# Performance work log

Hardware: AMD Instinct MI355X
Metric: run time of the kernel (lower is better)

The kernel has to match this reference:

```python
import jax, jax.numpy as jnp
import numpy as np

S, B, HID, NH = 256, 2, 512, 8
HD = HID // NH
C = 1.0            # Poincare ball curvature c (geoopt k = -c)
SQC = C ** 0.5
EPS = 1e-15


def _artanh(x):
    return jnp.arctanh(jnp.clip(x, -1 + 1e-7, 1 - 1e-7))


def artan_k(x):
    return _artanh(SQC * x) / SQC


def tan_k(x):
    return jnp.tanh(SQC * x) / SQC


def mobius_add(x, y):
    x2 = jnp.sum(x * x, -1, keepdims=True)
    y2 = jnp.sum(y * y, -1, keepdims=True)
    xy = jnp.sum(x * y, -1, keepdims=True)
    num = (1 + 2 * C * xy + C * y2) * x + (1 - C * x2) * y
    den = 1 + 2 * C * xy + C * C * x2 * y2
    return num / jnp.maximum(den, EPS)


def mobius_matvec(W, x):
    x_norm = jnp.maximum(jnp.linalg.norm(x, axis=-1, keepdims=True), EPS)
    mx = x @ W.T
    mx_norm = jnp.maximum(jnp.linalg.norm(mx, axis=-1, keepdims=True), EPS)
    res = tan_k(mx_norm / x_norm * artan_k(x_norm)) * (mx / mx_norm)
    zero = jnp.all(mx == 0, axis=-1, keepdims=True)
    return jnp.where(zero, 0.0, res)


def projx(x):
    n = jnp.maximum(jnp.linalg.norm(x, axis=-1, keepdims=True), EPS)
    maxnorm = (1 - 4e-3) / SQC  # float32 eps in geoopt
    return jnp.where(n > maxnorm, x / n * maxnorm, x)


def expmap0(u):
    n = jnp.maximum(jnp.linalg.norm(u, axis=-1, keepdims=True), EPS)
    return tan_k(n) * u / n


def logmap0(y):
    n = jnp.maximum(jnp.linalg.norm(y, axis=-1, keepdims=True), EPS)
    return artan_k(n) * y / n


def mobius_scalar_mul(r, x):
    n = jnp.maximum(jnp.linalg.norm(x, axis=-1, keepdims=True), EPS)
    return tan_k(r * artan_k(n)) * x / n


def manifold_linear(W, b, x):
    return projx(mobius_add(mobius_matvec(W, x), b))


def setup_inputs() -> dict:
    key = jax.random.key(0)
    ks = jax.random.split(key, 7)
    q = jax.random.normal(ks[0], (S, B, HID), jnp.float32) * 0.02
    w = lambda k: jax.random.normal(k, (HID, HID), jnp.float32) * 0.02
    bias = lambda k: jax.random.normal(k, (HID,), jnp.float32) * 0.01
    return {"query": q,
            "Wq": w(ks[1]), "bq": bias(ks[2]),
            "Wk": w(ks[3]), "bk": bias(ks[4]),
            "Wv": w(ks[5]), "bv": bias(ks[6])}


def reference(query, Wq, bq, Wk, bk, Wv, bv):
    x = jnp.transpose(query, (1, 0, 2))  # [B,S,HID], key=value=query
    Bn, Sn, _ = x.shape
    q = manifold_linear(Wq, bq, x)
    k = manifold_linear(Wk, bk, x)
    v = manifold_linear(Wv, bv, x)
    # faithful to torch .view(-1, H, S, D): plain memory reshape (not transpose)
    ql = expmap0(logmap0(q).reshape(Bn, NH, Sn, HD))
    kl = expmap0(logmap0(k).reshape(Bn, NH, Sn, HD))
    vl = expmap0(logmap0(v).reshape(Bn, NH, Sn, HD))
    # pairwise mobius_add(-q, k) -> [B,H,Q,N,D]; torch norm(p=-2) over D (faithful)
    diff = mobius_add(-ql[:, :, :, None, :], kl[:, :, None, :, :])
    t1 = jnp.sum(jnp.maximum(diff * diff, 1e-30) ** -1.0, axis=-1) ** -0.5
    scores = jnp.clip(-2.0 * artan_k(t1), -1e10, 1e10)
    probs = jax.nn.sigmoid(scores)  # [B,H,Q,N]; dropout p=0 -> identity
    # weighted gyro-midpoint over N (geoopt _weighted_midpoint, reducedim=[-1])
    gamma = 2.0 / jnp.maximum(1.0 - C * jnp.sum(vl * vl, -1), EPS)  # [B,H,N]
    denom = jnp.einsum('bhqn,bhn->bhq', probs, gamma - 1.0)
    sgn = jnp.where(denom >= 0, 1.0, -1.0)
    denom = sgn * jnp.maximum(jnp.abs(denom), 1e-10)
    nom = jnp.einsum('bhqn,bhnd->bhqd', probs, gamma[..., None] * vl)
    ctx = mobius_scalar_mul(0.5, nom / denom[..., None])  # [B,H,Q,D]
    ctx = jnp.transpose(ctx, (0, 2, 1, 3))  # [B,Q,H,D]
    ctx = expmap0(logmap0(ctx).reshape(Bn, Sn, HID))
    return jnp.transpose(ctx, (1, 0, 2)), probs
```

## Files before the change

### kernel.cpp

```cpp
#include <hip/hip_runtime.h>
#include <math.h>

constexpr int S_   = 256;
constexpr int B_   = 2;
constexpr int HID_ = 512;
constexpr int NH_  = 8;
constexpr int HD_  = 64;
constexpr int BSH  = B_ * S_ * HID_;


typedef unsigned short u16;
typedef short s16x8 __attribute__((ext_vector_type(8)));
typedef float f32x4 __attribute__((ext_vector_type(4)));

__device__ __forceinline__ float artanh_c(float x) {
    x = fminf(fmaxf(x, -0.9999999f), 0.9999999f);
    return 0.5f * __logf((1.f + x) / (1.f - x));
}

__device__ __forceinline__ float wsum64(float v) {
    #pragma unroll
    for (int o = 1; o < 64; o <<= 1) v += __shfl_xor(v, o, 64);
    return v;
}

__device__ __forceinline__ float block_sum_256(float v, float* red) {
    const int t = threadIdx.x;
    __syncthreads();
    red[t] = v;
    __syncthreads();
    #pragma unroll
    for (int sft = 128; sft > 0; sft >>= 1) {
        if (t < sft) red[t] += red[t + sft];
        __syncthreads();
    }
    return red[0];
}

__device__ __forceinline__ void split8(const float* v, s16x8& hi, s16x8& lo) {
    #pragma unroll
    for (int j = 0; j < 8; ++j) {
        const unsigned u = __float_as_uint(v[j]);
        const float hf = __uint_as_float(u & 0xFFFF0000u);
        hi[j] = (short)(u >> 16);
        lo[j] = (short)(__float_as_uint(v[j] - hf) >> 16);
    }
}

__global__ __launch_bounds__(256) void gemm3_fused_kernel(
    const float* __restrict__ query,
    const float* __restrict__ Wq, const float* __restrict__ Wk,
    const float* __restrict__ Wv, float* __restrict__ ws_mx)
{
    const int tid = threadIdx.x;
    const int rt = blockIdx.x >> 3;
    const int ct = blockIdx.x & 7;
    const int which = (rt * 32) >> 9;
    const int rloc  = (rt * 32) & 511;
    const float* __restrict__ W = (which == 0) ? Wq : (which == 1) ? Wk : Wv;

    __shared__ __align__(16) u16 sA[2][2][32 * 64];
    __shared__ __align__(16) u16 sB[2][2][64 * 64];

    const int ra = tid >> 3, sa = tid & 7;
    const int rb = tid >> 2, hb = (tid & 3) * 2;
    const int axrow = rloc + ra;
    const float* gA = query + (size_t)((axrow & 255) * 2 + (axrow >> 8)) * HID_ + sa * 8;
    const float* gB = W + (size_t)(ct * 64 + rb) * HID_ + hb * 8;
    const int wA  = ra * 64 + ((sa ^ (ra & 7)) * 8);
    const int wB0 = rb * 64 + ((hb ^ (rb & 7)) * 8);
    const int wB1 = rb * 64 + (((hb + 1) ^ (rb & 7)) * 8);

    const int lane = tid & 63, wv = tid >> 6;
    const int fr = lane & 15, fs = lane >> 4;
    const int aB0 = fr * 64,        ax0 = fr & 7;
    const int aB1 = (16 + fr) * 64, ax1 = (16 + fr) & 7;
    const int bB  = (wv * 16 + fr) * 64, bx = (wv * 16 + fr) & 7;

    float a8[8], b16[16];
    f32x4 acc[2] = {(f32x4){0.f,0.f,0.f,0.f}, (f32x4){0.f,0.f,0.f,0.f}};

#define G3_LOAD(c)  do { \
        const int k0 = (c) * 64; \
        *(float4*)&a8[0]  = *(const float4*)(gA + k0); \
        *(float4*)&a8[4]  = *(const float4*)(gA + k0 + 4); \
        *(float4*)&b16[0] = *(const float4*)(gB + k0); \
        *(float4*)&b16[4] = *(const float4*)(gB + k0 + 4); \
        *(float4*)&b16[8] = *(const float4*)(gB + k0 + 8); \
        *(float4*)&b16[12]= *(const float4*)(gB + k0 + 12); \
    } while (0)

#define G3_WRITE(b) do { \
        s16x8 h_, l_; \
        split8(a8, h_, l_); \
        *(s16x8*)&sA[b][0][wA] = h_;  *(s16x8*)&sA[b][1][wA] = l_; \
        split8(&b16[0], h_, l_); \
        *(s16x8*)&sB[b][0][wB0] = h_; *(s16x8*)&sB[b][1][wB0] = l_; \
        split8(&b16[8], h_, l_); \
        *(s16x8*)&sB[b][0][wB1] = h_; *(s16x8*)&sB[b][1][wB1] = l_; \
    } while (0)

    G3_LOAD(0);
    G3_WRITE(0);

    for (int c = 0; c < 8; ++c) {
        const int p = c & 1;
        __syncthreads();
        if (c < 7) G3_LOAD(c + 1);
        #pragma unroll
        for (int h = 0; h < 2; ++h) {
            const int sl = h * 4 + fs;
            s16x8 ah0 = *(const s16x8*)&sA[p][0][aB0 + ((sl ^ ax0) * 8)];
            s16x8 al0 = *(const s16x8*)&sA[p][1][aB0 + ((sl ^ ax0) * 8)];
            s16x8 ah1 = *(const s16x8*)&sA[p][0][aB1 + ((sl ^ ax1) * 8)];
            s16x8 al1 = *(const s16x8*)&sA[p][1][aB1 + ((sl ^ ax1) * 8)];
            s16x8 bh  = *(const s16x8*)&sB[p][0][bB  + ((sl ^ bx)  * 8)];
            s16x8 bl  = *(const s16x8*)&sB[p][1][bB  + ((sl ^ bx)  * 8)];
            acc[0] = __builtin_amdgcn_mfma_f32_16x16x32_bf16(ah0, bh, acc[0], 0, 0, 0);
            acc[0] = __builtin_amdgcn_mfma_f32_16x16x32_bf16(ah0, bl, acc[0], 0, 0, 0);
            acc[0] = __builtin_amdgcn_mfma_f32_16x16x32_bf16(al0, bh, acc[0], 0, 0, 0);
            acc[1] = __builtin_amdgcn_mfma_f32_16x16x32_bf16(ah1, bh, acc[1], 0, 0, 0);
            acc[1] = __builtin_amdgcn_mfma_f32_16x16x32_bf16(ah1, bl, acc[1], 0, 0, 0);
            acc[1] = __builtin_amdgcn_mfma_f32_16x16x32_bf16(al1, bh, acc[1], 0, 0, 0);
        }
        if (c < 7) G3_WRITE((c + 1) & 1);
    }
#undef G3_LOAD
#undef G3_WRITE

    #pragma unroll
    for (int i = 0; i < 2; ++i)
        #pragma unroll
        for (int q = 0; q < 4; ++q)
            ws_mx[(size_t)(rt * 32 + i * 16 + fs * 4 + q) * HID_ + ct * 64 + wv * 16 + fr]
                = acc[i][q];
}

__global__ __launch_bounds__(256) void mobius_rows_kernel(
    const float* __restrict__ query,
    const float* __restrict__ bq, const float* __restrict__ bk,
    const float* __restrict__ bv,
    float* __restrict__ ws_qkv, float* __restrict__ ws_gamma)
{
    const int lane = threadIdx.x & 63;
    const int wv   = threadIdx.x >> 6;
    const int row  = blockIdx.x * 4 + wv;
    const int which = row >> 9;
    const int rr    = row & 511;
    const float* __restrict__ bias = (which == 0) ? bq : (which == 1) ? bk : bv;
    float* mrow = ws_qkv + (size_t)row * HID_;
    const float* xrow = query + (size_t)((rr & 255) * 2 + (rr >> 8)) * HID_;

    float m[8], x[8], bb[8];
    *(float4*)&m[0]  = ((const float4*)mrow)[lane * 2];
    *(float4*)&m[4]  = ((const float4*)mrow)[lane * 2 + 1];
    *(float4*)&x[0]  = ((const float4*)xrow)[lane * 2];
    *(float4*)&x[4]  = ((const float4*)xrow)[lane * 2 + 1];
    *(float4*)&bb[0] = ((const float4*)bias)[lane * 2];
    *(float4*)&bb[4] = ((const float4*)bias)[lane * 2 + 1];

    float x2p = 0.f, m2p = 0.f, b2p = 0.f;
    #pragma unroll
    for (int j = 0; j < 8; ++j) {
        x2p = fmaf(x[j], x[j], x2p);
        m2p = fmaf(m[j], m[j], m2p);
        b2p = fmaf(bb[j], bb[j], b2p);
    }
    const float x2s = wsum64(x2p);
    const float mn2 = wsum64(m2p);
    const float b2s = wsum64(b2p);
    const float xn = fmaxf(sqrtf(x2s), 1e-15f);
    const float mn = fmaxf(sqrtf(mn2), 1e-15f);
    const float fac = tanhf(mn / xn * artanh_c(xn)) / mn;
    float r[8];
    float r2p = 0.f, ryp = 0.f;
    #pragma unroll
    for (int j = 0; j < 8; ++j) {
        r[j] = fac * m[j];
        r2p = fmaf(r[j], r[j], r2p);
        ryp = fmaf(r[j], bb[j], ryp);
    }
    const float r2s = wsum64(r2p);
    const float ry  = wsum64(ryp);
    const float a_c = 1.f + 2.f * ry + b2s;
    const float b_c = 1.f - r2s;
    const float den = 1.f + 2.f * ry + r2s * b2s;
    const float inv_den = 1.f / fmaxf(den, 1e-15f);
    float h[8];
    float h2p = 0.f;
    #pragma unroll
    for (int j = 0; j < 8; ++j) {
        h[j] = (a_c * r[j] + b_c * bb[j]) * inv_den;
        h2p = fmaf(h[j], h[j], h2p);
    }
    const float h2s = wsum64(h2p);
    float hn = fmaxf(sqrtf(h2s), 1e-15f);
    float pf = 1.f;
    if (hn > 0.996f) { pf = 0.996f / hn; hn = 0.996f; }
    const float lf = artanh_c(hn) / hn * pf;
    float l[8];
    float l2p = 0.f;
    #pragma unroll
    for (int j = 0; j < 8; ++j) {
        l[j] = lf * h[j];
        l2p = fmaf(l[j], l[j], l2p);
    }
    float cs = l2p;
    cs += __shfl_xor(cs, 1, 64);
    cs += __shfl_xor(cs, 2, 64);
    cs += __shfl_xor(cs, 4, 64);
    const float cn = fmaxf(sqrtf(cs), 1e-15f);
    const float th = tanhf(cn);
    const float sc = th / cn;
    float o[8];
    #pragma unroll
    for (int j = 0; j < 8; ++j) o[j] = sc * l[j];
    ((float4*)mrow)[lane * 2]     = *(float4*)&o[0];
    ((float4*)mrow)[lane * 2 + 1] = *(float4*)&o[4];
    if (which == 2 && (lane & 7) == 0) {
        const int j = lane >> 3;
        ws_gamma[(size_t)rr * NH_ + j] = 2.f / fmaxf(1.f - th * th, 1e-15f);
    }
}

__global__ __launch_bounds__(512, 4) void attn_kernel(
    const float* __restrict__ ws_qkv, const float* __restrict__ gamma,
    float* __restrict__ probs, float* __restrict__ lc)
{
    const int tid = threadIdx.x;
    const int bh  = blockIdx.x >> 5;
    const int q0  = (blockIdx.x & 31) * 8;
    const float* __restrict__ ql = ws_qkv + (size_t)bh * (S_ * HD_);
    const float* __restrict__ kl = ws_qkv + (size_t)BSH + (size_t)bh * (S_ * HD_);
    const float* __restrict__ vl = ws_qkv + (size_t)2 * BSH + (size_t)bh * (S_ * HD_);

    __shared__ __align__(16) float kS[128 * 64];
    __shared__ __align__(16) float qS[8 * 64];
    __shared__ __align__(16) float pS[8 * 256];
    __shared__ float gS[S_];
    __shared__ float k2S[128];
    __shared__ float nomP[8][8][64];
    __shared__ float dnS[8];

    if (tid < 256) gS[tid] = gamma[(size_t)bh * S_ + tid];
    if (tid < 128) ((float4*)qS)[tid] = ((const float4*)(ql + (size_t)q0 * 64))[tid];
    __syncthreads();

    const int lane = tid & 63;
    const int q_l  = tid >> 6;
    const int n_i  = lane & 31;
    const int dh   = lane >> 5;
    const int d0   = dh * 32;

    float qv[32];
    #pragma unroll
    for (int c = 0; c < 8; ++c)
        *(float4*)&qv[c * 4] = *(const float4*)&qS[q_l * 64 + d0 + c * 4];
    float q2p = 0.f;
    #pragma unroll
    for (int d = 0; d < 32; ++d) q2p = fmaf(qv[d], qv[d], q2p);
    const float q2 = q2p + __shfl_xor(q2p, 32, 64);
    const float b_c = 1.f - q2;
    float* __restrict__ prow = probs + ((size_t)(bh * S_ + q0 + q_l)) * S_;

    const int c4 = tid & 15;
    const int nb = tid >> 4;
    float sp = 0.f, spg = 0.f;

    for (int half = 0; half < 2; ++half) {
        __syncthreads();
        #pragma unroll
        for (int jj = 0; jj < 4; ++jj) {
            const int n = nb + 32 * jj;
            const float4 v = *(const float4*)(kl + ((size_t)(half * 128 + n)) * 64 + c4 * 4);
            *(float4*)&kS[n * 64 + ((c4 ^ (n & 15)) * 4)] = v;
            float pk = fmaf(v.x, v.x, fmaf(v.y, v.y, fmaf(v.z, v.z, v.w * v.w)));
            pk += __shfl_xor(pk, 1, 64);
            pk += __shfl_xor(pk, 2, 64);
            pk += __shfl_xor(pk, 4, 64);
            pk += __shfl_xor(pk, 8, 64);
            if (c4 == 0) k2S[n] = pk;
        }
        __syncthreads();
        #pragma unroll
        for (int j = 0; j < 4; ++j) {
            const int n = n_i + 32 * j;
            float kv[32];
            #pragma unroll
            for (int c = 0; c < 8; ++c) {
                const int sl = dh * 8 + c;
                *(float4*)&kv[c * 4] = *(const float4*)&kS[n * 64 + ((sl ^ (n & 15)) * 4)];
            }
            float s0 = 0.f, s1 = 0.f;
            #pragma unroll
            for (int d = 0; d < 32; d += 2) {
                s0 = fmaf(qv[d],     kv[d],     s0);
                s1 = fmaf(qv[d + 1], kv[d + 1], s1);
            }
            float s = s0 + s1;
            s += __shfl_xor(s, 32, 64);
            const float k2  = k2S[n];
            const float a_c = 1.f - 2.f * s + k2;
            const float den = fmaxf(fmaf(q2, k2, 1.f - 2.f * s), 1e-15f);
            const float ra  = __builtin_amdgcn_rcpf(a_c);
            const float r_c = b_c * ra;
            const float scale = den * den * ra * ra;
            const float c2  = 1e-30f * scale;
            float isA = 0.f, isB = 0.f;
            #pragma unroll
            for (int g = 0; g < 8; g += 2) {
                {
                    const int bse = g * 4;
                    const float w0 = fmaf(r_c, kv[bse + 0], -qv[bse + 0]);
                    const float w1 = fmaf(r_c, kv[bse + 1], -qv[bse + 1]);
                    const float w2 = fmaf(r_c, kv[bse + 2], -qv[bse + 2]);
                    const float w3 = fmaf(r_c, kv[bse + 3], -qv[bse + 3]);
                    const float ga = fmaf(w0, w0, c2), gb = fmaf(w1, w1, c2);
                    const float gc = fmaf(w2, w2, c2), gd = fmaf(w3, w3, c2);
                    const float pab = ga * gb, pcd = gc * gd;
                    const float num = fmaf(ga + gb, pcd, (gc + gd) * pab);
                    isA = fmaf(num, __builtin_amdgcn_rcpf(pab * pcd), isA);
                }
                {
                    const int bse = (g + 1) * 4;
                    const float w0 = fmaf(r_c, kv[bse + 0], -qv[bse + 0]);
                    const float w1 = fmaf(r_c, kv[bse + 1], -qv[bse + 1]);
                    const float w2 = fmaf(r_c, kv[bse + 2], -qv[bse + 2]);
                    const float w3 = fmaf(r_c, kv[bse + 3], -qv[bse + 3]);
                    const float ga = fmaf(w0, w0, c2), gb = fmaf(w1, w1, c2);
                    const float gc = fmaf(w2, w2, c2), gd = fmaf(w3, w3, c2);
                    const float pab = ga * gb, pcd = gc * gd;
                    const float num = fmaf(ga + gb, pcd, (gc + gd) * pab);
                    isB = fmaf(num, __builtin_amdgcn_rcpf(pab * pcd), isB);
                }
            }
            float invsum = isA + isB;
            invsum += __shfl_xor(invsum, 32, 64);
            const float t1 = __builtin_amdgcn_rsqf(scale * invsum);
            const float p = 0.5f - 0.5f * fminf(t1, 0.9999999f);
            const int gn = half * 128 + n;
            if (dh == 0) {
                prow[gn] = p;
                const float g = gS[gn];
                pS[q_l * 256 + gn] = p * g;
                sp += p; spg += p * g;
            }
        }
    }
    sp  = wsum64(sp);
    spg = wsum64(spg);
    if (lane == 0) dnS[q_l] = spg - sp;
    __syncthreads();

    const int w = q_l, d = lane;
    float acc[8] = {};
    const float* __restrict__ vbase = vl + (size_t)(w * 32) * 64;
    #pragma unroll
    for (int i4 = 0; i4 < 8; ++i4) {
        float vv[4];
        #pragma unroll
        for (int j2 = 0; j2 < 4; ++j2) vv[j2] = vbase[(size_t)(i4 * 4 + j2) * 64 + d];
        #pragma unroll
        for (int qq = 0; qq < 8; ++qq) {
            const float4 pq = *(const float4*)&pS[qq * 256 + w * 32 + i4 * 4];
            acc[qq] = fmaf(pq.x, vv[0], acc[qq]);
            acc[qq] = fmaf(pq.y, vv[1], acc[qq]);
            acc[qq] = fmaf(pq.z, vv[2], acc[qq]);
            acc[qq] = fmaf(pq.w, vv[3], acc[qq]);
        }
    }
    #pragma unroll
    for (int qq = 0; qq < 8; ++qq) nomP[w][qq][d] = acc[qq];
    __syncthreads();

    {
        const int qq = q_l;
        float nom = 0.f;
        #pragma unroll
        for (int w2 = 0; w2 < 8; ++w2) nom += nomP[w2][qq][d];
        const float dd = dnS[qq];
        const float adn = fmaxf(fabsf(dd), 1e-10f);
        const float sden = (dd >= 0.f) ? adn : -adn;
        const float m = nom / sden;
        const float ss = wsum64(m * m);
        const float nn = fmaxf(sqrtf(ss), 1e-15f);
        const float s1 = tanhf(0.5f * artanh_c(nn));
        const float res = s1 * m / nn;
        const float nres = fmaxf(s1, 1e-15f);
        lc[((size_t)(bh * S_ + q0 + qq)) * HD_ + d] = (artanh_c(nres) / nres) * res;
    }
}

__global__ __launch_bounds__(256) void outproj_kernel(
    const float* __restrict__ lc, float* __restrict__ out0)
{
    const int t = threadIdx.x;
    const int s = blockIdx.x & (S_ - 1);
    const int b = blockIdx.x >> 8;
    __shared__ float red[256];
    const int h0 = t >> 6, d0 = t & 63;
    const int e1 = t + 256;
    const int h1 = e1 >> 6, d1 = e1 & 63;
    const float v0 = lc[(((size_t)(b * NH_ + h0)) * S_ + s) * HD_ + d0];
    const float v1 = lc[(((size_t)(b * NH_ + h1)) * S_ + s) * HD_ + d1];
    const float ss = block_sum_256(v0 * v0 + v1 * v1, red);
    const float nn = fmaxf(sqrtf(ss), 1e-15f);
    const float f = tanhf(nn) / nn;
    float* orow = out0 + ((size_t)(s * B_ + b)) * HID_;
    orow[t] = f * v0;
    orow[t + 256] = f * v1;
}

extern "C" void kernel_launch(void* const* d_in, const int* in_sizes, int n_in,
                              void* d_out, int out_size, void* d_ws, size_t ws_size,
                              hipStream_t stream) {
    (void)in_sizes; (void)n_in; (void)out_size; (void)ws_size;
    const float* query = (const float*)d_in[0];
    const float* Wq = (const float*)d_in[1];
    const float* bq = (const float*)d_in[2];
    const float* Wk = (const float*)d_in[3];
    const float* bk = (const float*)d_in[4];
    const float* Wv = (const float*)d_in[5];
    const float* bv = (const float*)d_in[6];

    float* out0  = (float*)d_out;
    float* probs = out0 + (size_t)S_ * B_ * HID_;

    float* ws       = (float*)d_ws;
    float* ws_qkv   = ws;
    float* ws_gamma = ws + (size_t)3 * BSH;
    float* ws_lc    = ws + (size_t)3 * BSH + 4096;

    gemm3_fused_kernel<<<dim3(384), dim3(256), 0, stream>>>(query, Wq, Wk, Wv, ws_qkv);
    mobius_rows_kernel<<<dim3(384), dim3(256), 0, stream>>>(query, bq, bk, bv, ws_qkv, ws_gamma);
    attn_kernel<<<dim3(512), dim3(512), 0, stream>>>(ws_qkv, ws_gamma, probs, ws_lc);
    outproj_kernel<<<dim3(B_ * S_), dim3(256), 0, stream>>>(ws_lc, out0);
}
```

Measured before the change: 105.2 us.

## Fuse mobius row epilogue into GEMM and outproj into attention via last-block counters

Replaces the separate mobius_rows and outproj launches with last-arriving-block epilogues: the GEMM block that finishes a row tile's eighth column tile runs the mobius/projection math for those 32 rows. The attention block that completes all eight heads for a query group computes the output normalization. This removes two kernel launches and their inter-kernel gaps, but adds a memset launch, atomics and threadfences, and serializes the epilogue work onto fewer blocks.

Result: slower. 270.0 us (+156.7%).

```diff
diff --git a/kernel.cpp b/kernel.cpp
--- a/kernel.cpp
+++ b/kernel.cpp
@@ -24,19 +24,6 @@
     return v;
 }
 
-__device__ __forceinline__ float block_sum_256(float v, float* red) {
-    const int t = threadIdx.x;
-    __syncthreads();
-    red[t] = v;
-    __syncthreads();
-    #pragma unroll
-    for (int sft = 128; sft > 0; sft >>= 1) {
-        if (t < sft) red[t] += red[t + sft];
-        __syncthreads();
-    }
-    return red[0];
-}
-
 __device__ __forceinline__ void split8(const float* v, s16x8& hi, s16x8& lo) {
     #pragma unroll
     for (int j = 0; j < 8; ++j) {
@@ -47,10 +34,13 @@
     }
 }
 
-__global__ __launch_bounds__(256) void gemm3_fused_kernel(
+__global__ __launch_bounds__(256) void gemm3_mobius_kernel(
     const float* __restrict__ query,
-    const float* __restrict__ Wq, const float* __restrict__ Wk,
-    const float* __restrict__ Wv, float* __restrict__ ws_mx)
+    const float* __restrict__ Wq, const float* __restrict__ bq,
+    const float* __restrict__ Wk, const float* __restrict__ bk,
+    const float* __restrict__ Wv, const float* __restrict__ bv,
+    float* __restrict__ ws_qkv, float* __restrict__ ws_gamma,
+    unsigned int* __restrict__ cnt)
 {
     const int tid = threadIdx.x;
     const int rt = blockIdx.x >> 3;
@@ -61,6 +51,7 @@
 
     __shared__ __align__(16) u16 sA[2][2][32 * 64];
     __shared__ __align__(16) u16 sB[2][2][64 * 64];
+    __shared__ unsigned int lastS;
 
     const int ra = tid >> 3, sa = tid & 7;
     const int rb = tid >> 2, hb = (tid & 3) * 2;
@@ -71,11 +62,11 @@
     const int wB0 = rb * 64 + ((hb ^ (rb & 7)) * 8);
     const int wB1 = rb * 64 + (((hb + 1) ^ (rb & 7)) * 8);
 
-    const int lane = tid & 63, wv = tid >> 6;
+    const int lane = tid & 63, wvg = tid >> 6;
     const int fr = lane & 15, fs = lane >> 4;
     const int aB0 = fr * 64,        ax0 = fr & 7;
     const int aB1 = (16 + fr) * 64, ax1 = (16 + fr) & 7;
-    const int bB  = (wv * 16 + fr) * 64, bx = (wv * 16 + fr) & 7;
+    const int bB  = (wvg * 16 + fr) * 64, bx = (wvg * 16 + fr) & 7;
 
     float a8[8], b16[16];
     f32x4 acc[2] = {(f32x4){0.f,0.f,0.f,0.f}, (f32x4){0.f,0.f,0.f,0.f}};
@@ -132,100 +123,105 @@
     for (int i = 0; i < 2; ++i)
         #pragma unroll
         for (int q = 0; q < 4; ++q)
-            ws_mx[(size_t)(rt * 32 + i * 16 + fs * 4 + q) * HID_ + ct * 64 + wv * 16 + fr]
+            ws_qkv[(size_t)(rt * 32 + i * 16 + fs * 4 + q) * HID_ + ct * 64 + wvg * 16 + fr]
                 = acc[i][q];
-}
-
-__global__ __launch_bounds__(256) void mobius_rows_kernel(
-    const float* __restrict__ query,
-    const float* __restrict__ bq, const float* __restrict__ bk,
-    const float* __restrict__ bv,
-    float* __restrict__ ws_qkv, float* __restrict__ ws_gamma)
-{
-    const int lane = threadIdx.x & 63;
-    const int wv   = threadIdx.x >> 6;
-    const int row  = blockIdx.x * 4 + wv;
-    const int which = row >> 9;
-    const int rr    = row & 511;
-    const float* __restrict__ bias = (which == 0) ? bq : (which == 1) ? bk : bv;
-    float* mrow = ws_qkv + (size_t)row * HID_;
-    const float* xrow = query + (size_t)((rr & 255) * 2 + (rr >> 8)) * HID_;
-
-    float m[8], x[8], bb[8];
-    *(float4*)&m[0]  = ((const float4*)mrow)[lane * 2];
-    *(float4*)&m[4]  = ((const float4*)mrow)[lane * 2 + 1];
-    *(float4*)&x[0]  = ((const float4*)xrow)[lane * 2];
-    *(float4*)&x[4]  = ((const float4*)xrow)[lane * 2 + 1];
-    *(float4*)&bb[0] = ((const float4*)bias)[lane * 2];
-    *(float4*)&bb[4] = ((const float4*)bias)[lane * 2 + 1];
-
-    float x2p = 0.f, m2p = 0.f, b2p = 0.f;
-    #pragma unroll
-    for (int j = 0; j < 8; ++j) {
-        x2p = fmaf(x[j], x[j], x2p);
-        m2p = fmaf(m[j], m[j], m2p);
-        b2p = fmaf(bb[j], bb[j], b2p);
-    }
-    const float x2s = wsum64(x2p);
-    const float mn2 = wsum64(m2p);
-    const float b2s = wsum64(b2p);
-    const float xn = fmaxf(sqrtf(x2s), 1e-15f);
-    const float mn = fmaxf(sqrtf(mn2), 1e-15f);
-    const float fac = tanhf(mn / xn * artanh_c(xn)) / mn;
-    float r[8];
-    float r2p = 0.f, ryp = 0.f;
-    #pragma unroll
-    for (int j = 0; j < 8; ++j) {
-        r[j] = fac * m[j];
-        r2p = fmaf(r[j], r[j], r2p);
-        ryp = fmaf(r[j], bb[j], ryp);
-    }
-    const float r2s = wsum64(r2p);
-    const float ry  = wsum64(ryp);
-    const float a_c = 1.f + 2.f * ry + b2s;
-    const float b_c = 1.f - r2s;
-    const float den = 1.f + 2.f * ry + r2s * b2s;
-    const float inv_den = 1.f / fmaxf(den, 1e-15f);
-    float h[8];
-    float h2p = 0.f;
-    #pragma unroll
-    for (int j = 0; j < 8; ++j) {
-        h[j] = (a_c * r[j] + b_c * bb[j]) * inv_den;
-        h2p = fmaf(h[j], h[j], h2p);
-    }
-    const float h2s = wsum64(h2p);
-    float hn = fmaxf(sqrtf(h2s), 1e-15f);
-    float pf = 1.f;
-    if (hn > 0.996f) { pf = 0.996f / hn; hn = 0.996f; }
-    const float lf = artanh_c(hn) / hn * pf;
-    float l[8];
-    float l2p = 0.f;
-    #pragma unroll
-    for (int j = 0; j < 8; ++j) {
-        l[j] = lf * h[j];
-        l2p = fmaf(l[j], l[j], l2p);
-    }
-    float cs = l2p;
-    cs += __shfl_xor(cs, 1, 64);
-    cs += __shfl_xor(cs, 2, 64);
-    cs += __shfl_xor(cs, 4, 64);
-    const float cn = fmaxf(sqrtf(cs), 1e-15f);
-    const float th = tanhf(cn);
-    const float sc = th / cn;
-    float o[8];
-    #pragma unroll
-    for (int j = 0; j < 8; ++j) o[j] = sc * l[j];
-    ((float4*)mrow)[lane * 2]     = *(float4*)&o[0];
-    ((float4*)mrow)[lane * 2 + 1] = *(float4*)&o[4];
-    if (which == 2 && (lane & 7) == 0) {
-        const int j = lane >> 3;
-        ws_gamma[(size_t)rr * NH_ + j] = 2.f / fmaxf(1.f - th * th, 1e-15f);
-    }
-}
-
-__global__ __launch_bounds__(512, 4) void attn_kernel(
+
+    __threadfence();
+    if (tid == 0) {
+        const unsigned int old = __hip_atomic_fetch_add(&cnt[rt], 1u,
+                                    __ATOMIC_ACQ_REL, __HIP_MEMORY_SCOPE_AGENT);
+        lastS = (old == 7u) ? 1u : 0u;
+    }
+    __syncthreads();
+    if (lastS == 0u) return;
+    __threadfence();
+
+    #pragma unroll 1
+    for (int i = 0; i < 8; ++i) {
+        const int row  = rt * 32 + wvg * 8 + i;
+        const int wch  = row >> 9;
+        const int rr   = row & 511;
+        const float* __restrict__ bias = (wch == 0) ? bq : (wch == 1) ? bk : bv;
+        float* mrow = ws_qkv + (size_t)row * HID_;
+        const float* xrow = query + (size_t)((rr & 255) * 2 + (rr >> 8)) * HID_;
+
+        float m[8], x[8], bb[8];
+        *(float4*)&m[0]  = ((const float4*)mrow)[lane * 2];
+        *(float4*)&m[4]  = ((const float4*)mrow)[lane * 2 + 1];
+        *(float4*)&x[0]  = ((const float4*)xrow)[lane * 2];
+        *(float4*)&x[4]  = ((const float4*)xrow)[lane * 2 + 1];
+        *(float4*)&bb[0] = ((const float4*)bias)[lane * 2];
+        *(float4*)&bb[4] = ((const float4*)bias)[lane * 2 + 1];
+
+        float x2p = 0.f, m2p = 0.f, b2p = 0.f;
+        #pragma unroll
+        for (int j = 0; j < 8; ++j) {
+            x2p = fmaf(x[j], x[j], x2p);
+            m2p = fmaf(m[j], m[j], m2p);
+            b2p = fmaf(bb[j], bb[j], b2p);
+        }
+        const float x2s = wsum64(x2p);
+        const float mn2 = wsum64(m2p);
+        const float b2s = wsum64(b2p);
+        const float xn = fmaxf(sqrtf(x2s), 1e-15f);
+        const float mn = fmaxf(sqrtf(mn2), 1e-15f);
+        const float fac = tanhf(mn / xn * artanh_c(xn)) / mn;
+        float r[8];
+        float r2p = 0.f, ryp = 0.f;
+        #pragma unroll
+        for (int j = 0; j < 8; ++j) {
+            r[j] = fac * m[j];
+            r2p = fmaf(r[j], r[j], r2p);
+            ryp = fmaf(r[j], bb[j], ryp);
+        }
+        const float r2s = wsum64(r2p);
+        const float ry  = wsum64(ryp);
+        const float a_c = 1.f + 2.f * ry + b2s;
+        const float b_c = 1.f - r2s;
+        const float den = 1.f + 2.f * ry + r2s * b2s;
+        const float inv_den = 1.f / fmaxf(den, 1e-15f);
+        float h[8];
+        float h2p = 0.f;
+        #pragma unroll
+        for (int j = 0; j < 8; ++j) {
+            h[j] = (a_c * r[j] + b_c * bb[j]) * inv_den;
+            h2p = fmaf(h[j], h[j], h2p);
+        }
+        const float h2s = wsum64(h2p);
+        float hn = fmaxf(sqrtf(h2s), 1e-15f);
+        float pf = 1.f;
+        if (hn > 0.996f) { pf = 0.996f / hn; hn = 0.996f; }
+        const float lf = artanh_c(hn) / hn * pf;
+        float l[8];
+        float l2p = 0.f;
+        #pragma unroll
+        for (int j = 0; j < 8; ++j) {
+            l[j] = lf * h[j];
+            l2p = fmaf(l[j], l[j], l2p);
+        }
+        float cs = l2p;
+        cs += __shfl_xor(cs, 1, 64);
+        cs += __shfl_xor(cs, 2, 64);
+        cs += __shfl_xor(cs, 4, 64);
+        const float cn = fmaxf(sqrtf(cs), 1e-15f);
+        const float th = tanhf(cn);
+        const float sc = th / cn;
+        float o[8];
+        #pragma unroll
+        for (int j = 0; j < 8; ++j) o[j] = sc * l[j];
+        ((float4*)mrow)[lane * 2]     = *(float4*)&o[0];
+        ((float4*)mrow)[lane * 2 + 1] = *(float4*)&o[4];
+        if (wch == 2 && (lane & 7) == 0) {
+            const int j = lane >> 3;
+            ws_gamma[(size_t)rr * NH_ + j] = 2.f / fmaxf(1.f - th * th, 1e-15f);
+        }
+    }
+}
+
+__global__ __launch_bounds__(512, 4) void attn_outproj_kernel(
     const float* __restrict__ ws_qkv, const float* __restrict__ gamma,
-    float* __restrict__ probs, float* __restrict__ lc)
+    float* __restrict__ probs, float* __restrict__ lc,
+    float* __restrict__ out0, unsigned int* __restrict__ cntA)
 {
     const int tid = threadIdx.x;
     const int bh  = blockIdx.x >> 5;
@@ -241,6 +237,7 @@
     __shared__ float k2S[128];
     __shared__ float nomP[8][8][64];
     __shared__ float dnS[8];
+    __shared__ unsigned int lastS;
 
     if (tid < 256) gS[tid] = gamma[(size_t)bh * S_ + tid];
     if (tid < 128) ((float4*)qS)[tid] = ((const float4*)(ql + (size_t)q0 * 64))[tid];
@@ -389,26 +386,39 @@
         const float nres = fmaxf(s1, 1e-15f);
         lc[((size_t)(bh * S_ + q0 + qq)) * HD_ + d] = (artanh_c(nres) / nres) * res;
     }
-}
-
-__global__ __launch_bounds__(256) void outproj_kernel(
-    const float* __restrict__ lc, float* __restrict__ out0)
-{
-    const int t = threadIdx.x;
-    const int s = blockIdx.x & (S_ - 1);
-    const int b = blockIdx.x >> 8;
-    __shared__ float red[256];
-    const int h0 = t >> 6, d0 = t & 63;
-    const int e1 = t + 256;
-    const int h1 = e1 >> 6, d1 = e1 & 63;
-    const float v0 = lc[(((size_t)(b * NH_ + h0)) * S_ + s) * HD_ + d0];
-    const float v1 = lc[(((size_t)(b * NH_ + h1)) * S_ + s) * HD_ + d1];
-    const float ss = block_sum_256(v0 * v0 + v1 * v1, red);
-    const float nn = fmaxf(sqrtf(ss), 1e-15f);
-    const float f = tanhf(nn) / nn;
-    float* orow = out0 + ((size_t)(s * B_ + b)) * HID_;
-    orow[t] = f * v0;
-    orow[t + 256] = f * v1;
+
+    __threadfence();
+    const int b = bh >> 3;
+    if (tid == 0) {
+        const unsigned int old = __hip_atomic_fetch_add(&cntA[b * 32 + (q0 >> 3)], 1u,
+                                    __ATOMIC_ACQ_REL, __HIP_MEMORY_SCOPE_AGENT);
+        lastS = (old == 7u) ? 1u : 0u;
+    }
+    __syncthreads();
+    if (lastS == 0u) return;
+    __threadfence();
+
+    {
+        const int g = tid >> 6, l = tid & 63;
+        const int s = q0 + g;
+        const int h = l >> 3, dv = (l & 7) * 8;
+        const float* src = lc + (((size_t)(b * NH_ + h)) * S_ + s) * HD_ + dv;
+        float v[8];
+        *(float4*)&v[0] = *(const float4*)src;
+        *(float4*)&v[4] = *(const float4*)(src + 4);
+        float pp = 0.f;
+        #pragma unroll
+        for (int j = 0; j < 8; ++j) pp = fmaf(v[j], v[j], pp);
+        const float ss = wsum64(pp);
+        const float nn = fmaxf(sqrtf(ss), 1e-15f);
+        const float f = tanhf(nn) / nn;
+        float* orow = out0 + ((size_t)(s * B_ + b)) * HID_ + l * 8;
+        float o[8];
+        #pragma unroll
+        for (int j = 0; j < 8; ++j) o[j] = f * v[j];
+        *(float4*)&orow[0] = *(float4*)&o[0];
+        *(float4*)&orow[4] = *(float4*)&o[4];
+    }
 }
 
 extern "C" void kernel_launch(void* const* d_in, const int* in_sizes, int n_in,
@@ -430,9 +440,12 @@
     float* ws_qkv   = ws;
     float* ws_gamma = ws + (size_t)3 * BSH;
     float* ws_lc    = ws + (size_t)3 * BSH + 4096;
-
-    gemm3_fused_kernel<<<dim3(384), dim3(256), 0, stream>>>(query, Wq, Wk, Wv, ws_qkv);
-    mobius_rows_kernel<<<dim3(384), dim3(256), 0, stream>>>(query, bq, bk, bv, ws_qkv, ws_gamma);
-    attn_kernel<<<dim3(512), dim3(512), 0, stream>>>(ws_qkv, ws_gamma, probs, ws_lc);
-    outproj_kernel<<<dim3(B_ * S_), dim3(256), 0, stream>>>(ws_lc, out0);
-}
+    unsigned int* cnt  = (unsigned int*)(ws_lc + 131072);
+    unsigned int* cntA = cnt + 48;
+
+    hipMemsetAsync(cnt, 0, 112 * sizeof(unsigned int), stream);
+    gemm3_mobius_kernel<<<dim3(384), dim3(256), 0, stream>>>(
+        query, Wq, bq, Wk, bk, Wv, bv, ws_qkv, ws_gamma, cnt);
+    attn_outproj_kernel<<<dim3(512), dim3(512), 0, stream>>>(
+        ws_qkv, ws_gamma, probs, ws_lc, out0, cntA);
+}
```
